# Optimization experiments

Hardware: AMD Instinct MI355X
Metric: run time of the kernel (lower is better)

Reference implementation:

```python
import jax, jax.numpy as jnp
import numpy as np

H = 1024        # hidden_size
NH = 16         # num_attention_heads
DH = H // NH    # head dim = 64
I = 4096        # intermediate_size
E = 8           # moe_num_experts
B, S = 2, 2048
EPS = 1e-12


def _ln(x, g, b):
    mu = jnp.mean(x, axis=-1, keepdims=True)
    var = jnp.mean(jnp.square(x - mu), axis=-1, keepdims=True)
    return (x - mu) * jax.lax.rsqrt(var + EPS) * g + b


def setup_inputs() -> dict:
    key = jax.random.key(0)
    ks = jax.random.split(key, 16)
    std = 0.02
    p = {
        "hidden_states": jax.random.normal(ks[0], (B, S, H), jnp.float32),
        "Wq": jax.random.normal(ks[1], (H, H), jnp.float32) * std,
        "bq": jnp.zeros((H,), jnp.float32),
        "Wk": jax.random.normal(ks[2], (H, H), jnp.float32) * std,
        "bk": jnp.zeros((H,), jnp.float32),
        "Wv": jax.random.normal(ks[3], (H, H), jnp.float32) * std,
        "bv": jnp.zeros((H,), jnp.float32),
        "Wao": jax.random.normal(ks[4], (H, H), jnp.float32) * std,
        "bao": jnp.zeros((H,), jnp.float32),
        "ln1_g": jnp.ones((H,), jnp.float32),
        "ln1_b": jnp.zeros((H,), jnp.float32),
        "router_w": jax.random.normal(ks[5], (H, E), jnp.float32) * std,
        "We": jax.random.normal(ks[6], (E, H, I), jnp.float32) * std,
        "be": jnp.zeros((E, I), jnp.float32),
        "Wo": jax.random.normal(ks[7], (I, H), jnp.float32) * std,
        "bo": jnp.zeros((H,), jnp.float32),
        "ln2_g": jnp.ones((H,), jnp.float32),
        "ln2_b": jnp.zeros((H,), jnp.float32),
    }
    return p


def reference(hidden_states, Wq, bq, Wk, bk, Wv, bv, Wao, bao, ln1_g, ln1_b,
              router_w, We, be, Wo, bo, ln2_g, ln2_b):
    x = hidden_states  # [B,S,H]

    def heads(t):  # [B,S,H] -> [B,NH,S,DH]
        return t.reshape(B, S, NH, DH).transpose(0, 2, 1, 3)

    q = heads(x @ Wq + bq)
    k = heads(x @ Wk + bk)
    v = heads(x @ Wv + bv)
    scores = jnp.einsum("bhqd,bhkd->bhqk", q, k) / jnp.sqrt(jnp.float32(DH))
    probs = jax.nn.softmax(scores, axis=-1)
    ctx = jnp.einsum("bhqk,bhkd->bhqd", probs, v)
    ctx = ctx.transpose(0, 2, 1, 3).reshape(B, S, H)
    attn_out = _ln(ctx @ Wao + bao + x, ln1_g, ln1_b)  # BertSelfOutput

    # ---- MoE FFN: top-1 routing, per-expert GELU MLP, shared output proj ----
    flat = attn_out.reshape(-1, H)              # [N,H]
    logits = flat @ router_w                    # [N,E]
    idx = jnp.argmax(logits, axis=-1)           # top-1 of softmax == argmax of logits
    inter = jnp.zeros((flat.shape[0], I), flat.dtype)
    for e in range(E):  # small fixed expert count
        h_e = jax.nn.gelu(flat @ We[e] + be[e], approximate=False)
        inter = jnp.where((idx == e)[:, None], h_e, inter)
    inter = inter.reshape(B, S, I)
    out = _ln(inter @ Wo + bo + attn_out, ln2_g, ln2_b)  # BertOutput
    return out
```

## Files before the change

### kernel.cpp

```cpp
#include <hip/hip_runtime.h>
#include <hip/hip_bf16.h>
#include <cstdint>

#define H_  1024
#define NH_ 16
#define DH_ 64
#define I_  4096
#define E_  8
#define B_  2
#define S_  2048
#define N_  4096
#define QKVLD 3072
#define LN_EPS 1e-12f

typedef __attribute__((ext_vector_type(4))) float f4;
typedef __attribute__((ext_vector_type(8))) short s8v;
typedef unsigned int u32;

__device__ __forceinline__ float bf2f(unsigned short u) {
  union { unsigned int i; float f; } c; c.i = ((unsigned int)u) << 16; return c.f;
}
__device__ __forceinline__ unsigned short f2bf(float f) {
  __hip_bfloat16 h = __float2bfloat16(f);
  return *reinterpret_cast<unsigned short*>(&h);
}
__device__ __forceinline__ u32 pack_bf2(float a, float b) {
  return (u32)f2bf(a) | ((u32)f2bf(b) << 16);
}
__device__ __forceinline__ float gelu_f(float x) {
  return 0.5f * x * (1.0f + erff(x * 0.70710678118f));
}
__device__ __forceinline__ void gload16(const void* g, void* l) {
  __builtin_amdgcn_global_load_lds(
      (const __attribute__((address_space(1))) void*)g,
      (__attribute__((address_space(3))) void*)l, 16, 0, 0);
}

__global__ __launch_bounds__(256) void cvt_bf16_kernel(
    const float* __restrict__ in, ushort* __restrict__ out, int n8)
{
  const int t = blockIdx.x * 256 + threadIdx.x;
  if (t >= n8) return;
  const f4 x0 = *(const f4*)(in + (size_t)t * 8);
  const f4 x1 = *(const f4*)(in + (size_t)t * 8 + 4);
  s8v o;
#pragma unroll
  for (int j = 0; j < 4; ++j) { o[j] = (short)f2bf(x0[j]); o[4 + j] = (short)f2bf(x1[j]); }
  *(s8v*)(out + (size_t)t * 8) = o;
}

__global__ __launch_bounds__(256) void transpose_cvt_kernel(
    const float* __restrict__ in, ushort* __restrict__ out, int R, int C)
{
  __shared__ float Ls[64][68];
  const size_t zo = (size_t)blockIdx.z * (size_t)R * C;
  const int bx = blockIdx.x << 6;
  const int by = blockIdx.y << 6;
  const int tid = threadIdx.x;
  const int lr = tid >> 4, lc4 = (tid & 15) << 2;
  const float* ip = in + zo + (size_t)(by + lr) * C + bx + lc4;
#pragma unroll
  for (int i = 0; i < 4; ++i)
    *(f4*)&Ls[lr + (i << 4)][lc4] = *(const f4*)(ip + (size_t)(i << 4) * C);
  __syncthreads();
  const int oc = tid >> 2, seg = (tid & 3) << 4;
  ushort* op = out + zo + (size_t)(bx + oc) * R + by + seg;
  s8v v0, v1;
#pragma unroll
  for (int j = 0; j < 8; ++j) {
    v0[j] = (short)f2bf(Ls[seg + j][oc]);
    v1[j] = (short)f2bf(Ls[seg + 8 + j][oc]);
  }
  *(s8v*)op = v0;
  *(s8v*)(op + 8) = v1;
}

__global__ void concat3_kernel(const float* a, const float* b, const float* c,
                               float* __restrict__ o)
{
  const int t = blockIdx.x * 256 + threadIdx.x;
  if (t < 1024) o[t] = a[t];
  else if (t < 2048) o[t] = b[t - 1024];
  else o[t] = c[t - 2048];
}

__global__ __launch_bounds__(256) void gather_kernel(
    const ushort* __restrict__ X, const int* __restrict__ lists,
    ushort* __restrict__ Xg)
{
  const int r = (blockIdx.x << 1) + (threadIdx.x >> 7);
  const int c = (threadIdx.x & 127) << 3;
  const int tok = lists[r];
  *(s8v*)&Xg[(size_t)r * H_ + c] = *(const s8v*)&X[(size_t)tok * H_ + c];
}

__global__ __launch_bounds__(512, 2) void gemm256_bf16_kernel(
    const ushort* __restrict__ A, const ushort* __restrict__ Bt,
    const float* __restrict__ bias, ushort* __restrict__ Cout,
    const int M, const int N, const int K)
{
  __shared__ __align__(16) ushort Asm[2][4][256][8];
  __shared__ __align__(16) ushort Bsm[2][4][256][8];
  const int tid = threadIdx.x, w = tid >> 6, l = tid & 63;
  const int lq = l & 15, g = l >> 4;
  const int wm = w >> 2, wn = w & 3;
  const int nbx = N >> 8;
  const int nwg = nbx * (M >> 8);
  int id = blockIdx.y * nbx + blockIdx.x;
  id = (id & 7) * (nwg >> 3) + (id >> 3);
  const int m0 = (id / nbx) << 8, n0 = (id % nbx) << 8;

  const bool isB = (w >= 4);
  const int ks = w & 3;
  const ushort* gb = isB ? (Bt + (size_t)(n0 + l) * K + (ks << 3))
                         : (A + (size_t)(m0 + l) * K + (ks << 3));
  const ushort* p0 = gb;
  const ushort* p1 = gb + (size_t)64 * K;
  const ushort* p2 = gb + (size_t)128 * K;
  const ushort* p3 = gb + (size_t)192 * K;

  f4 acc[8][4] = {};
  const int nt = K >> 5;
#define STG(tt, buf) { const int kt_ = (tt) << 5;                          \
    ushort* d = isB ? &Bsm[buf][ks][0][0] : &Asm[buf][ks][0][0];           \
    gload16(p0 + kt_, d);          gload16(p1 + kt_, d + 64 * 8);          \
    gload16(p2 + kt_, d + 128 * 8); gload16(p3 + kt_, d + 192 * 8); }
  STG(0, 0);
  STG(1, 1);
  for (int t = 0; t < nt; ++t) {
    const int cur = t & 1;
    if (t + 1 < nt) { asm volatile("s_waitcnt vmcnt(4)" ::: "memory"); }
    else            { asm volatile("s_waitcnt vmcnt(0)" ::: "memory"); }
    __builtin_amdgcn_s_barrier();
    __builtin_amdgcn_sched_barrier(0);
    s8v af[8], bfv[4];
#pragma unroll
    for (int mi = 0; mi < 8; ++mi)
      af[mi] = *(const s8v*)&Asm[cur][g][(wm << 7) + (mi << 4) + lq][0];
#pragma unroll
    for (int ni = 0; ni < 4; ++ni)
      bfv[ni] = *(const s8v*)&Bsm[cur][g][(wn << 6) + (ni << 4) + lq][0];
    asm volatile("s_waitcnt lgkmcnt(0)" ::: "memory");
    __builtin_amdgcn_sched_barrier(0);
    __builtin_amdgcn_s_barrier();
    __builtin_amdgcn_sched_barrier(0);
    if (t + 2 < nt) STG(t + 2, cur);
#pragma unroll
    for (int mi = 0; mi < 8; ++mi)
#pragma unroll
      for (int ni = 0; ni < 4; ++ni)
        acc[mi][ni] = __builtin_amdgcn_mfma_f32_16x16x32_bf16(af[mi], bfv[ni], acc[mi][ni], 0, 0, 0);
  }
#undef STG
  __syncthreads();
  ushort* st = (ushort*)Asm + (size_t)w * (16 * 72);
  float bs[4];
#pragma unroll
  for (int ni = 0; ni < 4; ++ni) bs[ni] = bias[n0 + (wn << 6) + (ni << 4) + lq];
#pragma unroll
  for (int mi = 0; mi < 8; ++mi) {
#pragma unroll
    for (int ni = 0; ni < 4; ++ni)
#pragma unroll
      for (int r = 0; r < 4; ++r)
        st[((g << 2) + r) * 72 + (ni << 4) + lq] = f2bf(acc[mi][ni][r] + bs[ni]);
#pragma unroll
    for (int q2 = 0; q2 < 2; ++q2) {
      const int r16 = l & 15, ch = (l >> 4) + (q2 << 2);
      const s8v vv = *(const s8v*)&st[r16 * 72 + (ch << 3)];
      *(s8v*)&Cout[(size_t)(m0 + (wm << 7) + (mi << 4) + r16) * N
                   + n0 + (wn << 6) + (ch << 3)] = vv;
    }
  }
}

__global__ __launch_bounds__(512, 2) void moe256_mfma_kernel(
    const ushort* __restrict__ Xg, const ushort* __restrict__ WeT,
    const float* __restrict__ be, const int* __restrict__ lists,
    const int* __restrict__ offs, const int* __restrict__ cnt,
    const int* __restrict__ tb, ushort* __restrict__ inter)
{
  __shared__ __align__(16) ushort Asm[2][4][256][8];
  __shared__ __align__(16) ushort Bsm[2][4][256][8];
  __shared__ int tokL[256];
  const int by = blockIdx.y;
  if (by >= tb[E_]) return;
  int e = 0;
#pragma unroll
  for (int t = 1; t < E_; ++t) if (by >= tb[t]) e = t;
  const int rt = by - tb[e];
  const int base = offs[e] + (rt << 8);
  const int nrows = cnt[e] - (rt << 8);
  const int tid = threadIdx.x;
  if (tid < 256) tokL[tid] = (tid < nrows) ? lists[base + tid] : -1;
  __syncthreads();
  const int w = tid >> 6, l = tid & 63;
  const int lq = l & 15, g = l >> 4;
  const int wm = w >> 2, wn = w & 3;
  const int n0 = blockIdx.x << 8;

  const bool isB = (w >= 4);
  const int ks = w & 3;
  const ushort* Wp = WeT + (size_t)e * I_ * H_;
  const ushort* p0;
  const ushort* p1;
  const ushort* p2;
  const ushort* p3;
  if (isB) {
    const ushort* gb = Wp + (size_t)(n0 + l) * H_ + (ks << 3);
    p0 = gb; p1 = gb + (size_t)64 * H_; p2 = gb + (size_t)128 * H_; p3 = gb + (size_t)192 * H_;
  } else {
    p0 = Xg + (size_t)min(base + l,       N_ - 1) * H_ + (ks << 3);
    p1 = Xg + (size_t)min(base + 64 + l,  N_ - 1) * H_ + (ks << 3);
    p2 = Xg + (size_t)min(base + 128 + l, N_ - 1) * H_ + (ks << 3);
    p3 = Xg + (size_t)min(base + 192 + l, N_ - 1) * H_ + (ks << 3);
  }

  f4 acc[8][4] = {};
#define STG(tt, buf) { const int kt_ = (tt) << 5;                          \
    ushort* d = isB ? &Bsm[buf][ks][0][0] : &Asm[buf][ks][0][0];           \
    gload16(p0 + kt_, d);          gload16(p1 + kt_, d + 64 * 8);          \
    gload16(p2 + kt_, d + 128 * 8); gload16(p3 + kt_, d + 192 * 8); }
  STG(0, 0);
  STG(1, 1);
  for (int t = 0; t < 32; ++t) {
    const int cur = t & 1;
    if (t + 1 < 32) { asm volatile("s_waitcnt vmcnt(4)" ::: "memory"); }
    else            { asm volatile("s_waitcnt vmcnt(0)" ::: "memory"); }
    __builtin_amdgcn_s_barrier();
    __builtin_amdgcn_sched_barrier(0);
    s8v af[8], bfv[4];
#pragma unroll
    for (int mi = 0; mi < 8; ++mi)
      af[mi] = *(const s8v*)&Asm[cur][g][(wm << 7) + (mi << 4) + lq][0];
#pragma unroll
    for (int ni = 0; ni < 4; ++ni)
      bfv[ni] = *(const s8v*)&Bsm[cur][g][(wn << 6) + (ni << 4) + lq][0];
    asm volatile("s_waitcnt lgkmcnt(0)" ::: "memory");
    __builtin_amdgcn_sched_barrier(0);
    __builtin_amdgcn_s_barrier();
    __builtin_amdgcn_sched_barrier(0);
    if (t + 2 < 32) STG(t + 2, cur);
#pragma unroll
    for (int mi = 0; mi < 8; ++mi)
#pragma unroll
      for (int ni = 0; ni < 4; ++ni)
        acc[mi][ni] = __builtin_amdgcn_mfma_f32_16x16x32_bf16(af[mi], bfv[ni], acc[mi][ni], 0, 0, 0);
  }
#undef STG
  __syncthreads();
  ushort* st = (ushort*)Asm + (size_t)w * (16 * 72);
  float bs[4];
#pragma unroll
  for (int ni = 0; ni < 4; ++ni)
    bs[ni] = be[(size_t)e * I_ + n0 + (wn << 6) + (ni << 4) + lq];
#pragma unroll
  for (int mi = 0; mi < 8; ++mi) {
#pragma unroll
    for (int ni = 0; ni < 4; ++ni)
#pragma unroll
      for (int r = 0; r < 4; ++r)
        st[((g << 2) + r) * 72 + (ni << 4) + lq] = f2bf(gelu_f(acc[mi][ni][r] + bs[ni]));
#pragma unroll
    for (int q2 = 0; q2 < 2; ++q2) {
      const int r16 = l & 15, ch = (l >> 4) + (q2 << 2);
      const int tok = tokL[(wm << 7) + (mi << 4) + r16];
      if (tok >= 0) {
        const s8v vv = *(const s8v*)&st[r16 * 72 + (ch << 3)];
        *(s8v*)&inter[(size_t)tok * I_ + n0 + (wn << 6) + (ch << 3)] = vv;
      }
    }
  }
}

template <bool BF16OUT, int KSPLIT>
__global__ __launch_bounds__(256, 3) void gemm_mfma_kernel(
    const ushort* __restrict__ A, const ushort* __restrict__ Bt,
    const float* __restrict__ bias, void* __restrict__ Cout,
    const int M, const int N, const int K)
{
  __shared__ __align__(16) ushort Asm[3][4][128][8];
  __shared__ __align__(16) ushort Bsm[3][4][128][8];
  const int tid = threadIdx.x;
  const int w = tid >> 6, l = tid & 63;
  const int lq = l & 15, g = l >> 4;
  const int wm = w >> 1, wn = w & 1;
  const int nbx = N >> 7;
  const int nwg = nbx * (M >> 7);
  int id = blockIdx.y * nbx + blockIdx.x;
  id = (id & 7) * (nwg >> 3) + (id >> 3);
  const int m0 = (id / nbx) << 7, n0 = (id % nbx) << 7;
  const int Kspan = K / KSPLIT;
  const int kbase = (KSPLIT > 1) ? blockIdx.z * Kspan : 0;

  const ushort* a0 = A + (size_t)(m0 + l) * K + kbase + (w << 3);
  const ushort* a1 = a0 + (size_t)64 * K;
  const ushort* b0 = Bt + (size_t)(n0 + l) * K + kbase + (w << 3);
  const ushort* b1 = b0 + (size_t)64 * K;

  f4 acc[4][4] = {};
  const int nt = Kspan >> 5;
#define STAGE_G(tt, buf)                                   \
  { const int kt_ = (tt) << 5;                             \
    gload16(a0 + kt_, &Asm[buf][w][0][0]);                 \
    gload16(a1 + kt_, &Asm[buf][w][64][0]);                \
    gload16(b0 + kt_, &Bsm[buf][w][0][0]);                 \
    gload16(b1 + kt_, &Bsm[buf][w][64][0]); }
  STAGE_G(0, 0);
  STAGE_G(1, 1);
  int cur = 0, nxt2 = 2;
  for (int t = 0; t < nt; ++t) {
    if (t + 1 < nt) { asm volatile("s_waitcnt vmcnt(4)" ::: "memory"); }
    else            { asm volatile("s_waitcnt vmcnt(0)" ::: "memory"); }
    __builtin_amdgcn_s_barrier();
    __builtin_amdgcn_sched_barrier(0);
    if (t + 2 < nt) STAGE_G(t + 2, nxt2);
    s8v af[4], bfv[4];
#pragma unroll
    for (int mi = 0; mi < 4; ++mi)
      af[mi] = *(const s8v*)&Asm[cur][g][(wm << 6) + (mi << 4) + lq][0];
#pragma unroll
    for (int ni = 0; ni < 4; ++ni)
      bfv[ni] = *(const s8v*)&Bsm[cur][g][(wn << 6) + (ni << 4) + lq][0];
    asm volatile("s_waitcnt lgkmcnt(0)" ::: "memory");
    __builtin_amdgcn_sched_barrier(0);
#pragma unroll
    for (int mi = 0; mi < 4; ++mi)
#pragma unroll
      for (int ni = 0; ni < 4; ++ni)
        acc[mi][ni] = __builtin_amdgcn_mfma_f32_16x16x32_bf16(af[mi], bfv[ni], acc[mi][ni], 0, 0, 0);
    cur = (cur == 2) ? 0 : cur + 1;
    nxt2 = (nxt2 == 2) ? 0 : nxt2 + 1;
  }
#undef STAGE_G
  if constexpr (BF16OUT) {
    __syncthreads();
    ushort* st = (ushort*)Asm + (size_t)w * (16 * 72);
    float bs[4];
#pragma unroll
    for (int ni = 0; ni < 4; ++ni) bs[ni] = bias[n0 + (wn << 6) + (ni << 4) + lq];
#pragma unroll
    for (int mi = 0; mi < 4; ++mi) {
#pragma unroll
      for (int ni = 0; ni < 4; ++ni)
#pragma unroll
        for (int r = 0; r < 4; ++r)
          st[((g << 2) + r) * 72 + (ni << 4) + lq] = f2bf(acc[mi][ni][r] + bs[ni]);
#pragma unroll
      for (int q2 = 0; q2 < 2; ++q2) {
        const int r16 = l & 15, ch = (l >> 4) + (q2 << 2);
        const s8v vv = *(const s8v*)&st[r16 * 72 + (ch << 3)];
        *(s8v*)&((ushort*)Cout)[(size_t)(m0 + (wm << 6) + (mi << 4) + r16) * N
                                + n0 + (wn << 6) + (ch << 3)] = vv;
      }
    }
  } else {
    float* outf = (float*)Cout + (size_t)blockIdx.z * M * N;
#pragma unroll
    for (int ni = 0; ni < 4; ++ni) {
      const int col = n0 + (wn << 6) + (ni << 4) + lq;
      const float bs = (KSPLIT == 1 || blockIdx.z == 0) ? bias[col] : 0.f;
#pragma unroll
      for (int mi = 0; mi < 4; ++mi) {
        const int row = m0 + (wm << 6) + (mi << 4) + (g << 2);
#pragma unroll
        for (int r = 0; r < 4; ++r)
          outf[(size_t)(row + r) * N + col] = acc[mi][ni][r] + bs;
      }
    }
  }
}

__global__ __launch_bounds__(256) void attn_mfma_kernel(
    const ushort* __restrict__ qkv, ushort* __restrict__ ctx)
{
  __shared__ __align__(16) ushort Ks[64 * 72];
  __shared__ __align__(16) ushort Vr[64 * 72];
  __shared__ __align__(16) ushort Vt[64 * 72];
  __shared__ __align__(16) ushort Ps[4][16 * 72];
  const int bid0 = blockIdx.x;
  const int bid  = ((bid0 & 7) << 7) + (bid0 >> 3);
  const int bh = bid >> 5, qt = bid & 31;
  const int b = bh >> 4, h = bh & 15;
  const int tid = threadIdx.x, w = tid >> 6, l = tid & 63;
  const int lq = l & 15, g = l >> 4;
  const size_t bS = (size_t)b * S_;
  const ushort* qb = qkv + bS * QKVLD + h * DH_;
  const ushort* kb = qb + 1024;
  const ushort* vb = qb + 2048;

  s8v qf0, qf1;
  {
    const ushort* qp = qb + (size_t)(qt * 64 + w * 16 + lq) * QKVLD;
    qf0 = *(const s8v*)(qp + (g << 3));
    qf1 = *(const s8v*)(qp + 32 + (g << 3));
  }

  f4 o0 = {0,0,0,0}, o1 = {0,0,0,0}, o2 = {0,0,0,0}, o3 = {0,0,0,0};
  float mrun = -3.0e38f, lrun = 0.f;

  const int skey = tid >> 2;
  const int sd   = (tid & 3) << 4;

  s8v kr0, kr1, vr0, vr1;
#define ALOAD(t_) {                                                        \
    const ushort* kp_ = kb + (size_t)((t_) * 64 + skey) * QKVLD + sd;      \
    kr0 = *(const s8v*)kp_; kr1 = *(const s8v*)(kp_ + 8);                  \
    const ushort* vp_ = vb + (size_t)((t_) * 64 + skey) * QKVLD + sd;      \
    vr0 = *(const s8v*)vp_; vr1 = *(const s8v*)(vp_ + 8); }
#define AWRITE() {                                                         \
    *(s8v*)&Ks[skey * 72 + sd]     = kr0;                                  \
    *(s8v*)&Ks[skey * 72 + sd + 8] = kr1;                                  \
    *(s8v*)&Vr[skey * 72 + sd]     = vr0;                                  \
    *(s8v*)&Vr[skey * 72 + sd + 8] = vr1; }

  ALOAD(0); AWRITE();
  ALOAD(1);

  for (int kt = 0; kt < 32; ++kt) {
    asm volatile("s_waitcnt lgkmcnt(0)" ::: "memory");
    __builtin_amdgcn_sched_barrier(0);
    __builtin_amdgcn_s_barrier();
    __builtin_amdgcn_sched_barrier(0);

    {
      s8v t0, t1;
#pragma unroll
      for (int j = 0; j < 8; ++j) {
        t0[j] = (short)Vr[(w * 16 + j) * 72 + l];
        t1[j] = (short)Vr[(w * 16 + 8 + j) * 72 + l];
      }
      *(s8v*)&Vt[l * 72 + w * 16]     = t0;
      *(s8v*)&Vt[l * 72 + w * 16 + 8] = t1;
    }

    float s[16];
    __builtin_amdgcn_s_setprio(1);
#pragma unroll
    for (int st = 0; st < 4; ++st) {
      f4 acc = {0, 0, 0, 0};
      const s8v ka0 = *(const s8v*)&Ks[(st * 16 + lq) * 72 + (g << 3)];
      const s8v ka1 = *(const s8v*)&Ks[(st * 16 + lq) * 72 + 32 + (g << 3)];
      acc = __builtin_amdgcn_mfma_f32_16x16x32_bf16(ka0, qf0, acc, 0, 0, 0);
      acc = __builtin_amdgcn_mfma_f32_16x16x32_bf16(ka1, qf1, acc, 0, 0, 0);
      s[st * 4 + 0] = acc[0] * 0.125f; s[st * 4 + 1] = acc[1] * 0.125f;
      s[st * 4 + 2] = acc[2] * 0.125f; s[st * 4 + 3] = acc[3] * 0.125f;
    }
    __builtin_amdgcn_s_setprio(0);

    float tmax = s[0];
#pragma unroll
    for (int i = 1; i < 16; ++i) tmax = fmaxf(tmax, s[i]);
    tmax = fmaxf(tmax, __shfl_xor(tmax, 16));
    tmax = fmaxf(tmax, __shfl_xor(tmax, 32));
    if (!__all(tmax - mrun <= 8.f)) {
      const float mnew  = fmaxf(mrun, tmax);
      const float alpha = __expf(mrun - mnew);
      f4 av;
      av[0] = __shfl(alpha, g * 4 + 0); av[1] = __shfl(alpha, g * 4 + 1);
      av[2] = __shfl(alpha, g * 4 + 2); av[3] = __shfl(alpha, g * 4 + 3);
      o0 *= av; o1 *= av; o2 *= av; o3 *= av;
      lrun *= alpha; mrun = mnew;
    }
    float psum = 0.f;
#pragma unroll
    for (int i = 0; i < 16; ++i) { s[i] = __expf(s[i] - mrun); psum += s[i]; }
    psum += __shfl_xor(psum, 16); psum += __shfl_xor(psum, 32);
    lrun += psum;

    {
      ushort* pw = &Ps[w][lq * 72];
#pragma unroll
      for (int st = 0; st < 4; ++st) {
        *(u32*)&pw[st * 16 + g * 4 + 0] = pack_bf2(s[st * 4 + 0], s[st * 4 + 1]);
        *(u32*)&pw[st * 16 + g * 4 + 2] = pack_bf2(s[st * 4 + 2], s[st * 4 + 3]);
      }
    }
    asm volatile("s_waitcnt lgkmcnt(0)" ::: "memory");
    __builtin_amdgcn_sched_barrier(0);
    __builtin_amdgcn_s_barrier();
    __builtin_amdgcn_sched_barrier(0);

    __builtin_amdgcn_s_setprio(1);
#pragma unroll
    for (int ks = 0; ks < 2; ++ks) {
      const int kof = ks * 32 + (g << 3);
      const s8v pa = *(const s8v*)&Ps[w][lq * 72 + kof];
      const s8v v0 = *(const s8v*)&Vt[( 0 + lq) * 72 + kof];
      const s8v v1 = *(const s8v*)&Vt[(16 + lq) * 72 + kof];
      const s8v v2 = *(const s8v*)&Vt[(32 + lq) * 72 + kof];
      const s8v v3 = *(const s8v*)&Vt[(48 + lq) * 72 + kof];
      o0 = __builtin_amdgcn_mfma_f32_16x16x32_bf16(pa, v0, o0, 0, 0, 0);
      o1 = __builtin_amdgcn_mfma_f32_16x16x32_bf16(pa, v1, o1, 0, 0, 0);
      o2 = __builtin_amdgcn_mfma_f32_16x16x32_bf16(pa, v2, o2, 0, 0, 0);
      o3 = __builtin_amdgcn_mfma_f32_16x16x32_bf16(pa, v3, o3, 0, 0, 0);
    }
    __builtin_amdgcn_s_setprio(0);

    if (kt + 1 < 32) AWRITE();
    if (kt + 2 < 32) ALOAD(kt + 2);
  }
#undef ALOAD
#undef AWRITE

  const float inv = 1.f / lrun;
#pragma unroll
  for (int r = 0; r < 4; ++r) {
    const float li = __shfl(inv, g * 4 + r);
    ushort* op = ctx + (bS + (size_t)(qt * 64 + w * 16 + g * 4 + r)) * H_ + h * DH_ + lq;
    op[0]  = f2bf(o0[r] * li);
    op[16] = f2bf(o1[r] * li);
    op[32] = f2bf(o2[r] * li);
    op[48] = f2bf(o3[r] * li);
  }
}

template <int P>
__global__ __launch_bounds__(256) void add_ln_kernel(
    const float* __restrict__ a, const float* __restrict__ r,
    const float* __restrict__ g, const float* __restrict__ bta,
    float* __restrict__ out, ushort* __restrict__ ob)
{
  const int row = blockIdx.x, tid = threadIdx.x;
  const size_t base = (size_t)row * H_;
  const float4 xr = *(const float4*)(r + base + (tid << 2));
  float4 x = xr;
#pragma unroll
  for (int pp = 0; pp < P; ++pp) {
    const float4 xa = *(const float4*)(a + (size_t)pp * N_ * H_ + base + (tid << 2));
    x.x += xa.x; x.y += xa.y; x.z += xa.z; x.w += xa.w;
  }
  float s  = x.x + x.y + x.z + x.w;
  float ss = x.x * x.x + x.y * x.y + x.z * x.z + x.w * x.w;
#pragma unroll
  for (int off = 1; off < 64; off <<= 1) { s += __shfl_xor(s, off); ss += __shfl_xor(ss, off); }
  __shared__ float red[8];
  const int w = tid >> 6, ln = tid & 63;
  if (ln == 0) { red[w] = s; red[4 + w] = ss; }
  __syncthreads();
  const float S  = red[0] + red[1] + red[2] + red[3];
  const float SS = red[4] + red[5] + red[6] + red[7];
  const float mu  = S * (1.f / 1024.f);
  const float var = fmaxf(SS * (1.f / 1024.f) - mu * mu, 0.f);
  const float inv = rsqrtf(var + LN_EPS);
  const float4 gg = *(const float4*)&g[tid << 2];
  const float4 bb = *(const float4*)&bta[tid << 2];
  float4 y;
  y.x = (x.x - mu) * inv * gg.x + bb.x;
  y.y = (x.y - mu) * inv * gg.y + bb.y;
  y.z = (x.z - mu) * inv * gg.z + bb.z;
  y.w = (x.w - mu) * inv * gg.w + bb.w;
  *(float4*)&out[base + (tid << 2)] = y;
  if (ob) {
    ushort4 u;
    u.x = f2bf(y.x); u.y = f2bf(y.y); u.z = f2bf(y.z); u.w = f2bf(y.w);
    *(ushort4*)&ob[base + (tid << 2)] = u;
  }
}

__global__ __launch_bounds__(64) void router_kernel(
    const float* __restrict__ x, const float* __restrict__ rw,
    int* __restrict__ idx, int* __restrict__ cnt)
{
  const int t = blockIdx.x, lane = threadIdx.x;
  float acc[8] = {0.f};
  for (int c = 0; c < H_; c += 64) {
    const float xv = x[(size_t)t * H_ + c + lane];
    const float* wr = rw + (size_t)(c + lane) * E_;
    const float4 w0 = *(const float4*)wr;
    const float4 w1 = *(const float4*)(wr + 4);
    acc[0] += xv * w0.x; acc[1] += xv * w0.y; acc[2] += xv * w0.z; acc[3] += xv * w0.w;
    acc[4] += xv * w1.x; acc[5] += xv * w1.y; acc[6] += xv * w1.z; acc[7] += xv * w1.w;
  }
#pragma unroll
  for (int e = 0; e < E_; ++e) {
    float s = acc[e];
#pragma unroll
    for (int off = 1; off < 64; off <<= 1) s += __shfl_xor(s, off);
    acc[e] = s;
  }
  if (lane == 0) {
    int be_ = 0; float bv = acc[0];
#pragma unroll
    for (int e = 1; e < E_; ++e) if (acc[e] > bv) { bv = acc[e]; be_ = e; }
    idx[t] = be_;
    atomicAdd(&cnt[be_], 1);
  }
}

__global__ void init_kernel(int* cnt) { if (threadIdx.x < E_) cnt[threadIdx.x] = 0; }

__global__ void scan_kernel(const int* __restrict__ cnt, int* __restrict__ offs,
                            int* __restrict__ cursor, int* __restrict__ tb)
{
  int o = 0, tt = 0;
  for (int e = 0; e < E_; ++e) {
    offs[e] = o; cursor[e] = o; tb[e] = tt;
    o += cnt[e]; tt += (cnt[e] + 255) >> 8;
  }
  tb[E_] = tt;
}

__global__ __launch_bounds__(256) void scatter_kernel(
    const int* __restrict__ idx, int* __restrict__ cursor, int* __restrict__ lists)
{
  const int t = blockIdx.x * 256 + threadIdx.x;
  if (t < N_) {
    const int e = idx[t];
    const int p = atomicAdd(&cursor[e], 1);
    lists[p] = t;
  }
}

extern "C" void kernel_launch(void* const* d_in, const int* in_sizes, int n_in,
                              void* d_out, int out_size, void* d_ws, size_t ws_size,
                              hipStream_t stream) {
  const float* x   = (const float*)d_in[0];
  const float* Wq  = (const float*)d_in[1];
  const float* bq  = (const float*)d_in[2];
  const float* Wk  = (const float*)d_in[3];
  const float* bk  = (const float*)d_in[4];
  const float* Wv  = (const float*)d_in[5];
  const float* bv  = (const float*)d_in[6];
  const float* Wao = (const float*)d_in[7];
  const float* bao = (const float*)d_in[8];
  const float* g1  = (const float*)d_in[9];
  const float* b1  = (const float*)d_in[10];
  const float* rw  = (const float*)d_in[11];
  const float* We  = (const float*)d_in[12];
  const float* be  = (const float*)d_in[13];
  const float* Wo  = (const float*)d_in[14];
  const float* bo  = (const float*)d_in[15];
  const float* g2  = (const float*)d_in[16];
  const float* b2  = (const float*)d_in[17];
  float* out = (float*)d_out;

  char* p = (char*)d_ws;
  int* idx    = (int*)p; p += (size_t)N_ * 4;
  int* cnt    = (int*)p; p += 8 * 4;
  int* offs   = (int*)p; p += 8 * 4;
  int* cursor = (int*)p; p += 8 * 4;
  int* tb     = (int*)p; p += 16 * 4;
  int* lists  = (int*)p; p += (size_t)N_ * 4;
  p = (char*)(((uintptr_t)p + 255) & ~(uintptr_t)255);
  const size_t NH = (size_t)N_ * H_;
  ushort* xb     = (ushort*)p; p += NH * 2;
  ushort* qkvb   = (ushort*)p;
  float*  woPart = (float*)p;  p += (size_t)N_ * QKVLD * 2;
  ushort* ctxb   = (ushort*)p; p += NH * 2;
  float*  attn   = (float*)p;  p += NH * 4;
  ushort* attnb  = (ushort*)p; p += NH * 2;
  ushort* interb = (ushort*)p;
  float*  aoPart = (float*)p;  p += (size_t)N_ * I_ * 2;
  ushort* WqkvT  = (ushort*)p; p += (size_t)QKVLD * H_ * 2;
  ushort* WaoT   = (ushort*)p; p += (size_t)H_ * H_ * 2;
  ushort* WoT    = (ushort*)p; p += (size_t)H_ * I_ * 2;
  ushort* WeT    = (ushort*)p; p += (size_t)E_ * I_ * H_ * 2;
  float*  bqkv   = (float*)p;  p += QKVLD * 4;
  ushort* Xg     = xb;

  const dim3 blk(256);

  init_kernel<<<1, 64, 0, stream>>>(cnt);
  cvt_bf16_kernel<<<(N_ * H_ / 8 + 255) / 256, blk, 0, stream>>>(x, xb, N_ * H_ / 8);
  concat3_kernel<<<QKVLD / 256, blk, 0, stream>>>(bq, bk, bv, bqkv);
  transpose_cvt_kernel<<<dim3(16, 16, 1), blk, 0, stream>>>(Wq, WqkvT, H_, H_);
  transpose_cvt_kernel<<<dim3(16, 16, 1), blk, 0, stream>>>(Wk, WqkvT + (size_t)1024 * H_, H_, H_);
  transpose_cvt_kernel<<<dim3(16, 16, 1), blk, 0, stream>>>(Wv, WqkvT + (size_t)2048 * H_, H_, H_);
  transpose_cvt_kernel<<<dim3(16, 16, 1), blk, 0, stream>>>(Wao, WaoT, H_, H_);
  transpose_cvt_kernel<<<dim3(16, 64, 1), blk, 0, stream>>>(Wo, WoT, I_, H_);
  transpose_cvt_kernel<<<dim3(64, 16, 8), blk, 0, stream>>>(We, WeT, H_, I_);

  gemm256_bf16_kernel<<<dim3(QKVLD / 256, N_ / 256), dim3(512), 0, stream>>>(
      xb, WqkvT, bqkv, qkvb, N_, QKVLD, H_);
  attn_mfma_kernel<<<1024, blk, 0, stream>>>(qkvb, ctxb);
  gemm_mfma_kernel<false, 2><<<dim3(H_ / 128, N_ / 128, 2), blk, 0, stream>>>(
      ctxb, WaoT, bao, aoPart, N_, H_, H_);
  add_ln_kernel<2><<<N_, blk, 0, stream>>>(aoPart, x, g1, b1, attn, attnb);
  router_kernel<<<N_, 64, 0, stream>>>(attn, rw, idx, cnt);
  scan_kernel<<<1, 1, 0, stream>>>(cnt, offs, cursor, tb);
  scatter_kernel<<<N_ / 256, blk, 0, stream>>>(idx, cursor, lists);
  gather_kernel<<<N_ / 2, blk, 0, stream>>>(attnb, lists, Xg);
  moe256_mfma_kernel<<<dim3(I_ / 256, N_ / 256 + E_), dim3(512), 0, stream>>>(
      Xg, WeT, be, lists, offs, cnt, tb, interb);
  gemm_mfma_kernel<false, 2><<<dim3(H_ / 128, N_ / 128, 2), blk, 0, stream>>>(
      interb, WoT, bo, woPart, N_, H_, I_);
  add_ln_kernel<2><<<N_, blk, 0, stream>>>(woPart, attn, g2, b2, out, (ushort*)nullptr);
}
```

Baseline: 516.6 us.

## Merge small launches and widen attention blocks to 128 queries

New measurement: 483.1 us. -6.5%, faster.

```diff
diff --git a/kernel.cpp b/kernel.cpp
--- a/kernel.cpp
+++ b/kernel.cpp
@@ -37,8 +37,9 @@
 }
 
 __global__ __launch_bounds__(256) void cvt_bf16_kernel(
-    const float* __restrict__ in, ushort* __restrict__ out, int n8)
-{
+    const float* __restrict__ in, ushort* __restrict__ out, int n8, int* __restrict__ cnt)
+{
+  if (blockIdx.x == 0 && threadIdx.x < E_) cnt[threadIdx.x] = 0;
   const int t = blockIdx.x * 256 + threadIdx.x;
   if (t >= n8) return;
   const f4 x0 = *(const f4*)(in + (size_t)t * 8);
@@ -49,22 +50,21 @@
   *(s8v*)(out + (size_t)t * 8) = o;
 }
 
-__global__ __launch_bounds__(256) void transpose_cvt_kernel(
+__device__ __forceinline__ void transpose_body(
     const float* __restrict__ in, ushort* __restrict__ out, int R, int C)
 {
   __shared__ float Ls[64][68];
-  const size_t zo = (size_t)blockIdx.z * (size_t)R * C;
   const int bx = blockIdx.x << 6;
   const int by = blockIdx.y << 6;
   const int tid = threadIdx.x;
   const int lr = tid >> 4, lc4 = (tid & 15) << 2;
-  const float* ip = in + zo + (size_t)(by + lr) * C + bx + lc4;
+  const float* ip = in + (size_t)(by + lr) * C + bx + lc4;
 #pragma unroll
   for (int i = 0; i < 4; ++i)
     *(f4*)&Ls[lr + (i << 4)][lc4] = *(const f4*)(ip + (size_t)(i << 4) * C);
   __syncthreads();
   const int oc = tid >> 2, seg = (tid & 3) << 4;
-  ushort* op = out + zo + (size_t)(bx + oc) * R + by + seg;
+  ushort* op = out + (size_t)(bx + oc) * R + by + seg;
   s8v v0, v1;
 #pragma unroll
   for (int j = 0; j < 8; ++j) {
@@ -73,6 +73,23 @@
   }
   *(s8v*)op = v0;
   *(s8v*)(op + 8) = v1;
+}
+
+__global__ __launch_bounds__(256) void transpose_cvt_kernel(
+    const float* __restrict__ in, ushort* __restrict__ out, int R, int C)
+{
+  transpose_body(in + (size_t)blockIdx.z * R * C, out + (size_t)blockIdx.z * R * C, R, C);
+}
+
+__global__ __launch_bounds__(256) void transpose_cvt4_kernel(
+    const float* __restrict__ s0, const float* __restrict__ s1,
+    const float* __restrict__ s2, const float* __restrict__ s3,
+    ushort* __restrict__ dqkv, ushort* __restrict__ dao)
+{
+  const int z = blockIdx.z;
+  const float* in = (z == 0) ? s0 : (z == 1) ? s1 : (z == 2) ? s2 : s3;
+  ushort* out = (z < 3) ? (dqkv + (size_t)z * H_ * H_) : dao;
+  transpose_body(in, out, H_, H_);
 }
 
 __global__ void concat3_kernel(const float* a, const float* b, const float* c,
@@ -84,6 +101,28 @@
   else o[t] = c[t - 2048];
 }
 
+__global__ __launch_bounds__(256) void scan_scatter_kernel(
+    const int* __restrict__ idx, const int* __restrict__ cnt,
+    int* __restrict__ offs, int* __restrict__ tb, int* __restrict__ lists)
+{
+  __shared__ int lcur[E_];
+  const int tid = threadIdx.x;
+  if (tid == 0) {
+    int o = 0, tt = 0;
+    for (int e = 0; e < E_; ++e) {
+      offs[e] = o; lcur[e] = o; tb[e] = tt;
+      o += cnt[e]; tt += (cnt[e] + 255) >> 8;
+    }
+    tb[E_] = tt;
+  }
+  __syncthreads();
+  for (int t = tid; t < N_; t += 256) {
+    const int e = idx[t];
+    const int p = atomicAdd(&lcur[e], 1);
+    lists[p] = t;
+  }
+}
+
 __global__ __launch_bounds__(256) void gather_kernel(
     const ushort* __restrict__ X, const int* __restrict__ lists,
     ushort* __restrict__ Xg)
@@ -94,7 +133,7 @@
   *(s8v*)&Xg[(size_t)r * H_ + c] = *(const s8v*)&X[(size_t)tok * H_ + c];
 }
 
-__global__ __launch_bounds__(512, 2) void gemm256_bf16_kernel(
+__global__ __launch_bounds__(512, 2) void gemm256_kernel(
     const ushort* __restrict__ A, const ushort* __restrict__ Bt,
     const float* __restrict__ bias, ushort* __restrict__ Cout,
     const int M, const int N, const int K)
@@ -170,6 +209,81 @@
       const s8v vv = *(const s8v*)&st[r16 * 72 + (ch << 3)];
       *(s8v*)&Cout[(size_t)(m0 + (wm << 7) + (mi << 4) + r16) * N
                    + n0 + (wn << 6) + (ch << 3)] = vv;
+    }
+  }
+}
+
+template <int KSPLIT>
+__global__ __launch_bounds__(256, 3) void gemm128_kernel(
+    const ushort* __restrict__ A, const ushort* __restrict__ Bt,
+    const float* __restrict__ bias, float* __restrict__ Cout,
+    const int M, const int N, const int K)
+{
+  __shared__ __align__(16) ushort Asm[3][4][128][8];
+  __shared__ __align__(16) ushort Bsm[3][4][128][8];
+  const int tid = threadIdx.x;
+  const int w = tid >> 6, l = tid & 63;
+  const int lq = l & 15, g = l >> 4;
+  const int wm = w >> 1, wn = w & 1;
+  const int nbx = N >> 7;
+  const int nwg = nbx * (M >> 7);
+  int id = blockIdx.y * nbx + blockIdx.x;
+  id = (id & 7) * (nwg >> 3) + (id >> 3);
+  const int m0 = (id / nbx) << 7, n0 = (id % nbx) << 7;
+  const int Kspan = K / KSPLIT;
+  const int kbase = (KSPLIT > 1) ? blockIdx.z * Kspan : 0;
+
+  const ushort* a0 = A + (size_t)(m0 + l) * K + kbase + (w << 3);
+  const ushort* a1 = a0 + (size_t)64 * K;
+  const ushort* b0 = Bt + (size_t)(n0 + l) * K + kbase + (w << 3);
+  const ushort* b1 = b0 + (size_t)64 * K;
+
+  f4 acc[4][4] = {};
+  const int nt = Kspan >> 5;
+#define STAGE_G(tt, buf)                                   \
+  { const int kt_ = (tt) << 5;                             \
+    gload16(a0 + kt_, &Asm[buf][w][0][0]);                 \
+    gload16(a1 + kt_, &Asm[buf][w][64][0]);                \
+    gload16(b0 + kt_, &Bsm[buf][w][0][0]);                 \
+    gload16(b1 + kt_, &Bsm[buf][w][64][0]); }
+  STAGE_G(0, 0);
+  STAGE_G(1, 1);
+  int cur = 0, nxt2 = 2;
+  for (int t = 0; t < nt; ++t) {
+    if (t + 1 < nt) { asm volatile("s_waitcnt vmcnt(4)" ::: "memory"); }
+    else            { asm volatile("s_waitcnt vmcnt(0)" ::: "memory"); }
+    __builtin_amdgcn_s_barrier();
+    __builtin_amdgcn_sched_barrier(0);
+    if (t + 2 < nt) STAGE_G(t + 2, nxt2);
+    s8v af[4], bfv[4];
+#pragma unroll
+    for (int mi = 0; mi < 4; ++mi)
+      af[mi] = *(const s8v*)&Asm[cur][g][(wm << 6) + (mi << 4) + lq][0];
+#pragma unroll
+    for (int ni = 0; ni < 4; ++ni)
+      bfv[ni] = *(const s8v*)&Bsm[cur][g][(wn << 6) + (ni << 4) + lq][0];
+    asm volatile("s_waitcnt lgkmcnt(0)" ::: "memory");
+    __builtin_amdgcn_sched_barrier(0);
+#pragma unroll
+    for (int mi = 0; mi < 4; ++mi)
+#pragma unroll
+      for (int ni = 0; ni < 4; ++ni)
+        acc[mi][ni] = __builtin_amdgcn_mfma_f32_16x16x32_bf16(af[mi], bfv[ni], acc[mi][ni], 0, 0, 0);
+    cur = (cur == 2) ? 0 : cur + 1;
+    nxt2 = (nxt2 == 2) ? 0 : nxt2 + 1;
+  }
+#undef STAGE_G
+  float* outf = Cout + (size_t)blockIdx.z * M * N;
+#pragma unroll
+  for (int ni = 0; ni < 4; ++ni) {
+    const int col = n0 + (wn << 6) + (ni << 4) + lq;
+    const float bs = (KSPLIT == 1 || blockIdx.z == 0) ? bias[col] : 0.f;
+#pragma unroll
+    for (int mi = 0; mi < 4; ++mi) {
+      const int row = m0 + (wm << 6) + (mi << 4) + (g << 2);
+#pragma unroll
+      for (int r = 0; r < 4; ++r)
+        outf[(size_t)(row + r) * N + col] = acc[mi][ni][r] + bs;
     }
   }
 }
@@ -273,114 +387,16 @@
   }
 }
 
-template <bool BF16OUT, int KSPLIT>
-__global__ __launch_bounds__(256, 3) void gemm_mfma_kernel(
-    const ushort* __restrict__ A, const ushort* __restrict__ Bt,
-    const float* __restrict__ bias, void* __restrict__ Cout,
-    const int M, const int N, const int K)
-{
-  __shared__ __align__(16) ushort Asm[3][4][128][8];
-  __shared__ __align__(16) ushort Bsm[3][4][128][8];
-  const int tid = threadIdx.x;
-  const int w = tid >> 6, l = tid & 63;
-  const int lq = l & 15, g = l >> 4;
-  const int wm = w >> 1, wn = w & 1;
-  const int nbx = N >> 7;
-  const int nwg = nbx * (M >> 7);
-  int id = blockIdx.y * nbx + blockIdx.x;
-  id = (id & 7) * (nwg >> 3) + (id >> 3);
-  const int m0 = (id / nbx) << 7, n0 = (id % nbx) << 7;
-  const int Kspan = K / KSPLIT;
-  const int kbase = (KSPLIT > 1) ? blockIdx.z * Kspan : 0;
-
-  const ushort* a0 = A + (size_t)(m0 + l) * K + kbase + (w << 3);
-  const ushort* a1 = a0 + (size_t)64 * K;
-  const ushort* b0 = Bt + (size_t)(n0 + l) * K + kbase + (w << 3);
-  const ushort* b1 = b0 + (size_t)64 * K;
-
-  f4 acc[4][4] = {};
-  const int nt = Kspan >> 5;
-#define STAGE_G(tt, buf)                                   \
-  { const int kt_ = (tt) << 5;                             \
-    gload16(a0 + kt_, &Asm[buf][w][0][0]);                 \
-    gload16(a1 + kt_, &Asm[buf][w][64][0]);                \
-    gload16(b0 + kt_, &Bsm[buf][w][0][0]);                 \
-    gload16(b1 + kt_, &Bsm[buf][w][64][0]); }
-  STAGE_G(0, 0);
-  STAGE_G(1, 1);
-  int cur = 0, nxt2 = 2;
-  for (int t = 0; t < nt; ++t) {
-    if (t + 1 < nt) { asm volatile("s_waitcnt vmcnt(4)" ::: "memory"); }
-    else            { asm volatile("s_waitcnt vmcnt(0)" ::: "memory"); }
-    __builtin_amdgcn_s_barrier();
-    __builtin_amdgcn_sched_barrier(0);
-    if (t + 2 < nt) STAGE_G(t + 2, nxt2);
-    s8v af[4], bfv[4];
-#pragma unroll
-    for (int mi = 0; mi < 4; ++mi)
-      af[mi] = *(const s8v*)&Asm[cur][g][(wm << 6) + (mi << 4) + lq][0];
-#pragma unroll
-    for (int ni = 0; ni < 4; ++ni)
-      bfv[ni] = *(const s8v*)&Bsm[cur][g][(wn << 6) + (ni << 4) + lq][0];
-    asm volatile("s_waitcnt lgkmcnt(0)" ::: "memory");
-    __builtin_amdgcn_sched_barrier(0);
-#pragma unroll
-    for (int mi = 0; mi < 4; ++mi)
-#pragma unroll
-      for (int ni = 0; ni < 4; ++ni)
-        acc[mi][ni] = __builtin_amdgcn_mfma_f32_16x16x32_bf16(af[mi], bfv[ni], acc[mi][ni], 0, 0, 0);
-    cur = (cur == 2) ? 0 : cur + 1;
-    nxt2 = (nxt2 == 2) ? 0 : nxt2 + 1;
-  }
-#undef STAGE_G
-  if constexpr (BF16OUT) {
-    __syncthreads();
-    ushort* st = (ushort*)Asm + (size_t)w * (16 * 72);
-    float bs[4];
-#pragma unroll
-    for (int ni = 0; ni < 4; ++ni) bs[ni] = bias[n0 + (wn << 6) + (ni << 4) + lq];
-#pragma unroll
-    for (int mi = 0; mi < 4; ++mi) {
-#pragma unroll
-      for (int ni = 0; ni < 4; ++ni)
-#pragma unroll
-        for (int r = 0; r < 4; ++r)
-          st[((g << 2) + r) * 72 + (ni << 4) + lq] = f2bf(acc[mi][ni][r] + bs[ni]);
-#pragma unroll
-      for (int q2 = 0; q2 < 2; ++q2) {
-        const int r16 = l & 15, ch = (l >> 4) + (q2 << 2);
-        const s8v vv = *(const s8v*)&st[r16 * 72 + (ch << 3)];
-        *(s8v*)&((ushort*)Cout)[(size_t)(m0 + (wm << 6) + (mi << 4) + r16) * N
-                                + n0 + (wn << 6) + (ch << 3)] = vv;
-      }
-    }
-  } else {
-    float* outf = (float*)Cout + (size_t)blockIdx.z * M * N;
-#pragma unroll
-    for (int ni = 0; ni < 4; ++ni) {
-      const int col = n0 + (wn << 6) + (ni << 4) + lq;
-      const float bs = (KSPLIT == 1 || blockIdx.z == 0) ? bias[col] : 0.f;
-#pragma unroll
-      for (int mi = 0; mi < 4; ++mi) {
-        const int row = m0 + (wm << 6) + (mi << 4) + (g << 2);
-#pragma unroll
-        for (int r = 0; r < 4; ++r)
-          outf[(size_t)(row + r) * N + col] = acc[mi][ni][r] + bs;
-      }
-    }
-  }
-}
-
-__global__ __launch_bounds__(256) void attn_mfma_kernel(
+__global__ __launch_bounds__(512) void attn_mfma_kernel(
     const ushort* __restrict__ qkv, ushort* __restrict__ ctx)
 {
   __shared__ __align__(16) ushort Ks[64 * 72];
   __shared__ __align__(16) ushort Vr[64 * 72];
   __shared__ __align__(16) ushort Vt[64 * 72];
-  __shared__ __align__(16) ushort Ps[4][16 * 72];
+  __shared__ __align__(16) ushort Ps[8][16 * 72];
   const int bid0 = blockIdx.x;
-  const int bid  = ((bid0 & 7) << 7) + (bid0 >> 3);
-  const int bh = bid >> 5, qt = bid & 31;
+  const int bid  = ((bid0 & 7) << 6) + (bid0 >> 3);
+  const int bh = bid >> 4, qt = bid & 15;
   const int b = bh >> 4, h = bh & 15;
   const int tid = threadIdx.x, w = tid >> 6, l = tid & 63;
   const int lq = l & 15, g = l >> 4;
@@ -391,7 +407,7 @@
 
   s8v qf0, qf1;
   {
-    const ushort* qp = qb + (size_t)(qt * 64 + w * 16 + lq) * QKVLD;
+    const ushort* qp = qb + (size_t)(qt * 128 + w * 16 + lq) * QKVLD;
     qf0 = *(const s8v*)(qp + (g << 3));
     qf1 = *(const s8v*)(qp + 32 + (g << 3));
   }
@@ -399,20 +415,16 @@
   f4 o0 = {0,0,0,0}, o1 = {0,0,0,0}, o2 = {0,0,0,0}, o3 = {0,0,0,0};
   float mrun = -3.0e38f, lrun = 0.f;
 
-  const int skey = tid >> 2;
-  const int sd   = (tid & 3) << 4;
-
-  s8v kr0, kr1, vr0, vr1;
+  const int skey = tid >> 3;
+  const int sd   = (tid & 7) << 3;
+
+  s8v kr0, vr0;
 #define ALOAD(t_) {                                                        \
-    const ushort* kp_ = kb + (size_t)((t_) * 64 + skey) * QKVLD + sd;      \
-    kr0 = *(const s8v*)kp_; kr1 = *(const s8v*)(kp_ + 8);                  \
-    const ushort* vp_ = vb + (size_t)((t_) * 64 + skey) * QKVLD + sd;      \
-    vr0 = *(const s8v*)vp_; vr1 = *(const s8v*)(vp_ + 8); }
+    kr0 = *(const s8v*)(kb + (size_t)((t_) * 64 + skey) * QKVLD + sd);     \
+    vr0 = *(const s8v*)(vb + (size_t)((t_) * 64 + skey) * QKVLD + sd); }
 #define AWRITE() {                                                         \
-    *(s8v*)&Ks[skey * 72 + sd]     = kr0;                                  \
-    *(s8v*)&Ks[skey * 72 + sd + 8] = kr1;                                  \
-    *(s8v*)&Vr[skey * 72 + sd]     = vr0;                                  \
-    *(s8v*)&Vr[skey * 72 + sd + 8] = vr1; }
+    *(s8v*)&Ks[skey * 72 + sd] = kr0;                                      \
+    *(s8v*)&Vr[skey * 72 + sd] = vr0; }
 
   ALOAD(0); AWRITE();
   ALOAD(1);
@@ -424,14 +436,11 @@
     __builtin_amdgcn_sched_barrier(0);
 
     {
-      s8v t0, t1;
-#pragma unroll
-      for (int j = 0; j < 8; ++j) {
-        t0[j] = (short)Vr[(w * 16 + j) * 72 + l];
-        t1[j] = (short)Vr[(w * 16 + 8 + j) * 72 + l];
-      }
-      *(s8v*)&Vt[l * 72 + w * 16]     = t0;
-      *(s8v*)&Vt[l * 72 + w * 16 + 8] = t1;
+      s8v t0;
+#pragma unroll
+      for (int j = 0; j < 8; ++j)
+        t0[j] = (short)Vr[(w * 8 + j) * 72 + l];
+      *(s8v*)&Vt[l * 72 + w * 8] = t0;
     }
 
     float s[16];
@@ -507,7 +516,7 @@
 #pragma unroll
   for (int r = 0; r < 4; ++r) {
     const float li = __shfl(inv, g * 4 + r);
-    ushort* op = ctx + (bS + (size_t)(qt * 64 + w * 16 + g * 4 + r)) * H_ + h * DH_ + lq;
+    ushort* op = ctx + (bS + (size_t)(qt * 128 + w * 16 + g * 4 + r)) * H_ + h * DH_ + lq;
     op[0]  = f2bf(o0[r] * li);
     op[16] = f2bf(o1[r] * li);
     op[32] = f2bf(o2[r] * li);
@@ -588,30 +597,6 @@
   }
 }
 
-__global__ void init_kernel(int* cnt) { if (threadIdx.x < E_) cnt[threadIdx.x] = 0; }
-
-__global__ void scan_kernel(const int* __restrict__ cnt, int* __restrict__ offs,
-                            int* __restrict__ cursor, int* __restrict__ tb)
-{
-  int o = 0, tt = 0;
-  for (int e = 0; e < E_; ++e) {
-    offs[e] = o; cursor[e] = o; tb[e] = tt;
-    o += cnt[e]; tt += (cnt[e] + 255) >> 8;
-  }
-  tb[E_] = tt;
-}
-
-__global__ __launch_bounds__(256) void scatter_kernel(
-    const int* __restrict__ idx, int* __restrict__ cursor, int* __restrict__ lists)
-{
-  const int t = blockIdx.x * 256 + threadIdx.x;
-  if (t < N_) {
-    const int e = idx[t];
-    const int p = atomicAdd(&cursor[e], 1);
-    lists[p] = t;
-  }
-}
-
 extern "C" void kernel_launch(void* const* d_in, const int* in_sizes, int n_in,
                               void* d_out, int out_size, void* d_ws, size_t ws_size,
                               hipStream_t stream) {
@@ -639,7 +624,6 @@
   int* idx    = (int*)p; p += (size_t)N_ * 4;
   int* cnt    = (int*)p; p += 8 * 4;
   int* offs   = (int*)p; p += 8 * 4;
-  int* cursor = (int*)p; p += 8 * 4;
   int* tb     = (int*)p; p += 16 * 4;
   int* lists  = (int*)p; p += (size_t)N_ * 4;
   p = (char*)(((uintptr_t)p + 255) & ~(uintptr_t)255);
@@ -660,30 +644,26 @@
   ushort* Xg     = xb;
 
   const dim3 blk(256);
-
-  init_kernel<<<1, 64, 0, stream>>>(cnt);
-  cvt_bf16_kernel<<<(N_ * H_ / 8 + 255) / 256, blk, 0, stream>>>(x, xb, N_ * H_ / 8);
+  const dim3 blk512(512);
+
+  cvt_bf16_kernel<<<(N_ * H_ / 8 + 255) / 256, blk, 0, stream>>>(x, xb, N_ * H_ / 8, cnt);
   concat3_kernel<<<QKVLD / 256, blk, 0, stream>>>(bq, bk, bv, bqkv);
-  transpose_cvt_kernel<<<dim3(16, 16, 1), blk, 0, stream>>>(Wq, WqkvT, H_, H_);
-  transpose_cvt_kernel<<<dim3(16, 16, 1), blk, 0, stream>>>(Wk, WqkvT + (size_t)1024 * H_, H_, H_);
-  transpose_cvt_kernel<<<dim3(16, 16, 1), blk, 0, stream>>>(Wv, WqkvT + (size_t)2048 * H_, H_, H_);
-  transpose_cvt_kernel<<<dim3(16, 16, 1), blk, 0, stream>>>(Wao, WaoT, H_, H_);
+  transpose_cvt4_kernel<<<dim3(16, 16, 4), blk, 0, stream>>>(Wq, Wk, Wv, Wao, WqkvT, WaoT);
   transpose_cvt_kernel<<<dim3(16, 64, 1), blk, 0, stream>>>(Wo, WoT, I_, H_);
   transpose_cvt_kernel<<<dim3(64, 16, 8), blk, 0, stream>>>(We, WeT, H_, I_);
 
-  gemm256_bf16_kernel<<<dim3(QKVLD / 256, N_ / 256), dim3(512), 0, stream>>>(
+  gemm256_kernel<<<dim3(QKVLD / 256, N_ / 256), blk512, 0, stream>>>(
       xb, WqkvT, bqkv, qkvb, N_, QKVLD, H_);
-  attn_mfma_kernel<<<1024, blk, 0, stream>>>(qkvb, ctxb);
-  gemm_mfma_kernel<false, 2><<<dim3(H_ / 128, N_ / 128, 2), blk, 0, stream>>>(
+  attn_mfma_kernel<<<512, blk512, 0, stream>>>(qkvb, ctxb);
+  gemm128_kernel<2><<<dim3(H_ / 128, N_ / 128, 2), blk, 0, stream>>>(
       ctxb, WaoT, bao, aoPart, N_, H_, H_);
   add_ln_kernel<2><<<N_, blk, 0, stream>>>(aoPart, x, g1, b1, attn, attnb);
   router_kernel<<<N_, 64, 0, stream>>>(attn, rw, idx, cnt);
-  scan_kernel<<<1, 1, 0, stream>>>(cnt, offs, cursor, tb);
-  scatter_kernel<<<N_ / 256, blk, 0, stream>>>(idx, cursor, lists);
+  scan_scatter_kernel<<<1, blk, 0, stream>>>(idx, cnt, offs, tb, lists);
   gather_kernel<<<N_ / 2, blk, 0, stream>>>(attnb, lists, Xg);
-  moe256_mfma_kernel<<<dim3(I_ / 256, N_ / 256 + E_), dim3(512), 0, stream>>>(
+  moe256_mfma_kernel<<<dim3(I_ / 256, N_ / 256 + E_), blk512, 0, stream>>>(
       Xg, WeT, be, lists, offs, cnt, tb, interb);
-  gemm_mfma_kernel<false, 2><<<dim3(H_ / 128, N_ / 128, 2), blk, 0, stream>>>(
+  gemm128_kernel<2><<<dim3(H_ / 128, N_ / 128, 2), blk, 0, stream>>>(
       interb, WoT, bo, woPart, N_, H_, I_);
   add_ln_kernel<2><<<N_, blk, 0, stream>>>(woPart, attn, g2, b2, out, (ushort*)nullptr);
 }
```
